# Kernel tuning notes

Hardware: AMD Instinct MI355X
Metric: run time of the kernel (lower is better)

The kernel has to match this reference:

```python
import jax, jax.numpy as jnp
import numpy as np

EMBED = 512
HEADS = 8
HEAD_DIM = EMBED // HEADS
N, S = 4, 2048


def setup_inputs() -> dict:
    key = jax.random.key(0)
    ks = jax.random.split(key, 10)
    value = jax.random.normal(ks[0], (N, S, EMBED), dtype=jnp.float32)
    k_in = jax.random.normal(ks[1], (N, S, EMBED), dtype=jnp.float32)
    q_in = jax.random.normal(ks[2], (N, S, EMBED), dtype=jnp.float32)
    mask = jax.random.randint(ks[3], (N, 1, S, S), 0, 2, dtype=jnp.int32)
    s = 1.0 / np.sqrt(HEAD_DIM)
    Wq = jax.random.uniform(ks[4], (HEAD_DIM, HEAD_DIM), minval=-s, maxval=s, dtype=jnp.float32)
    Wk = jax.random.uniform(ks[5], (HEAD_DIM, HEAD_DIM), minval=-s, maxval=s, dtype=jnp.float32)
    Wv = jax.random.uniform(ks[6], (HEAD_DIM, HEAD_DIM), minval=-s, maxval=s, dtype=jnp.float32)
    so = 1.0 / np.sqrt(EMBED)
    Wo = jax.random.uniform(ks[7], (EMBED, EMBED), minval=-so, maxval=so, dtype=jnp.float32)
    bo = jax.random.uniform(ks[8], (EMBED,), minval=-so, maxval=so, dtype=jnp.float32)
    return {"value": value, "key": k_in, "query": q_in, "mask": mask,
            "Wq": Wq, "Wk": Wk, "Wv": Wv, "Wo": Wo, "bo": bo}


def reference(value, key, query, mask, Wq, Wk, Wv, Wo, bo):
    n, qlen = query.shape[0], query.shape[1]
    # split heads: (N, L, H, D)
    v = value.reshape(n, -1, HEADS, HEAD_DIM)
    k = key.reshape(n, -1, HEADS, HEAD_DIM)
    q = query.reshape(n, qlen, HEADS, HEAD_DIM)
    # per-head linear projections (torch Linear: x @ W^T, no bias)
    v = jnp.einsum('nlhd,ed->nlhe', v, Wv)
    k = jnp.einsum('nlhd,ed->nlhe', k, Wk)
    q = jnp.einsum('nqhd,ed->nqhe', q, Wq)
    # energy: (N, H, Q, K)
    energy = jnp.einsum('nqhd,nkhd->nhqk', q, k)
    energy = jnp.where(mask == 0, jnp.float32(-1e20), energy)
    # NOTE: original scales by sqrt(embed_size), not sqrt(head_dim)
    attn = jax.nn.softmax(energy / jnp.sqrt(jnp.float32(EMBED)), axis=3)
    out = jnp.einsum('nhql,nlhd->nqhd', attn, v).reshape(n, qlen, EMBED)
    return out @ Wo.T + bo
```

## Files before the change

### kernel.cpp

```cpp
#include <hip/hip_runtime.h>

typedef short short8 __attribute__((ext_vector_type(8)));
typedef float f32x4 __attribute__((ext_vector_type(4)));
typedef unsigned short ushort4v __attribute__((ext_vector_type(4)));
typedef unsigned long long u64;
typedef u64 u64x2 __attribute__((ext_vector_type(2)));

#define N_B   4
#define S_LEN 2048
#define EMB   512
#define HD    64
#define NHB   32
#define QSCALE 0.063758714f

#define EXP2F(x) __builtin_amdgcn_exp2f(x)

__device__ unsigned short g_Wqb[64*64];
__device__ unsigned short g_Wkb[64*64];
__device__ unsigned short g_Wvb[64*64];
__device__ unsigned short g_Wob[512*512];
__device__ unsigned short g_Qp[NHB*S_LEN*HD];
__device__ unsigned short g_Kp[NHB*S_LEN*HD];
__device__ unsigned short g_Vt[NHB*HD*S_LEN];
__device__ unsigned short g_AO[N_B*S_LEN*EMB];
__device__ u64            g_Mb[N_B*32*S_LEN];

__device__ __forceinline__ unsigned short f2bf(float f) {
  unsigned u = __float_as_uint(f);
  u = u + 0x7fffu + ((u >> 16) & 1u);
  return (unsigned short)(u >> 16);
}

__device__ __forceinline__ unsigned cvt_pk_bf16(float a, float b) {
  unsigned r;
  asm("v_cvt_pk_bf16_f32 %0, %1, %2" : "=v"(r) : "v"(a), "v"(b));
  return r;
}

__global__ __launch_bounds__(256) void k0_wconv(const float* __restrict__ Wq,
                                                const float* __restrict__ Wk,
                                                const float* __restrict__ Wv,
                                                const float* __restrict__ Wo) {
  int idx = blockIdx.x * 256 + threadIdx.x;
  if (idx < 4096)        g_Wqb[idx]         = f2bf(Wq[idx] * QSCALE);
  else if (idx < 8192)   g_Wkb[idx - 4096]  = f2bf(Wk[idx - 4096]);
  else if (idx < 12288)  g_Wvb[idx - 8192]  = f2bf(Wv[idx - 8192]);
  else                   g_Wob[idx - 12288] = f2bf(Wo[idx - 12288]);
}

__global__ __launch_bounds__(256) void k0b_mask(const int* __restrict__ mask) {
  int wid = blockIdx.x * 4 + (threadIdx.x >> 6);
  int lane = threadIdx.x & 63;
  int n = wid >> 11, q = wid & 2047;
  const int* base = mask + ((size_t)(n * 2048 + q) << 11);
  u64* dst = g_Mb + (size_t)n * 32 * S_LEN + q;
#pragma unroll 4
  for (int j = 0; j < 32; ++j) {
    int mk = base[j * 64 + lane];
    u64 bits = __ballot(mk != 0);
    if (lane == 0) dst[(size_t)j * S_LEN] = bits;
  }
}

__global__ __launch_bounds__(256) void k1_proj(const float* __restrict__ q_in,
                                               const float* __restrict__ k_in,
                                               const float* __restrict__ v_in) {
  __shared__ unsigned short VtL[64][72];
  const int tid = threadIdx.x;
  const int w = tid >> 6, lane = tid & 63, g = lane >> 4, c = lane & 15;
  const int s0 = blockIdx.x * 64;
  const int nh = blockIdx.y, n = nh >> 3, h = nh & 7;
  const int which = blockIdx.z;
  const float* src = which == 0 ? q_in : (which == 1 ? k_in : v_in);
  const unsigned short* Wb = which == 0 ? g_Wqb : (which == 1 ? g_Wkb : g_Wvb);

  short8 xb[2];
  const int srow = s0 + w * 16 + c;
#pragma unroll
  for (int ks = 0; ks < 2; ++ks) {
    const float* ap = src + ((size_t)n * S_LEN + srow) * EMB + h * HD + ks * 32 + g * 8;
    f32x4 x0 = *(const f32x4*)ap;
    f32x4 x1 = *(const f32x4*)(ap + 4);
    short8 tt;
    tt[0] = (short)f2bf(x0[0]); tt[1] = (short)f2bf(x0[1]);
    tt[2] = (short)f2bf(x0[2]); tt[3] = (short)f2bf(x0[3]);
    tt[4] = (short)f2bf(x1[0]); tt[5] = (short)f2bf(x1[1]);
    tt[6] = (short)f2bf(x1[2]); tt[7] = (short)f2bf(x1[3]);
    xb[ks] = tt;
  }

  f32x4 acc[4];
#pragma unroll
  for (int dt = 0; dt < 4; ++dt) { acc[dt][0]=0.f; acc[dt][1]=0.f; acc[dt][2]=0.f; acc[dt][3]=0.f; }

#pragma unroll
  for (int ks = 0; ks < 2; ++ks)
#pragma unroll
    for (int dt = 0; dt < 4; ++dt) {
      short8 a = *(const short8*)(Wb + (dt * 16 + c) * HD + ks * 32 + g * 8);
      acc[dt] = __builtin_amdgcn_mfma_f32_16x16x32_bf16(a, xb[ks], acc[dt], 0, 0, 0);
    }

  if (which < 2) {
    unsigned short* dst = which == 0 ? g_Qp : g_Kp;
#pragma unroll
    for (int dt = 0; dt < 4; ++dt) {
      ushort4v u;
      u[0] = f2bf(acc[dt][0]); u[1] = f2bf(acc[dt][1]);
      u[2] = f2bf(acc[dt][2]); u[3] = f2bf(acc[dt][3]);
      *(ushort4v*)(dst + ((size_t)nh * S_LEN + srow) * HD + dt * 16 + 4 * g) = u;
    }
  } else {
#pragma unroll
    for (int dt = 0; dt < 4; ++dt)
#pragma unroll
      for (int r = 0; r < 4; ++r)
        VtL[dt * 16 + 4 * g + r][w * 16 + c] = f2bf(acc[dt][r]);
    __syncthreads();
#pragma unroll
    for (int rep = 0; rep < 2; ++rep) {
      int cid = tid + rep * 256;
      int row = cid >> 3, ch = cid & 7;
      short8 v = *(const short8*)(&VtL[row][ch * 8]);
      *(short8*)(g_Vt + ((size_t)nh * HD + row) * S_LEN + s0 + ch * 8) = v;
    }
  }
}

__global__ __launch_bounds__(512) void k2_attn() {
  __shared__ unsigned short Kl[2][64][64];
  __shared__ unsigned short Vl[2][80][64];
  __shared__ unsigned short Pl[8][16][64];
  const int tid = threadIdx.x;
  const int w = tid >> 6, lane = tid & 63, g = lane >> 4, c = lane & 15;
  const int q0 = blockIdx.x * 128;
  const int nh = blockIdx.y, n = nh >> 3;

  short8 aq[2];
#pragma unroll
  for (int ks = 0; ks < 2; ++ks)
    aq[ks] = *(const short8*)(g_Qp + ((size_t)nh * S_LEN + q0 + w * 16 + c) * HD + ks * 32 + g * 8);

  const int strow = tid >> 3, schunk = tid & 7;
  const int sdst = (schunk ^ (strow & 7)) * 8;
  const unsigned short* ksrc = g_Kp + ((size_t)nh * S_LEN + strow) * HD + schunk * 8;
  const unsigned short* vsrc = g_Vt + ((size_t)nh * HD + strow) * S_LEN + schunk * 8;
  const u64* mbase = g_Mb + ((size_t)n * 32) * S_LEN + q0 + w * 16 + 4 * g;

  {
    int flat = tid * 4;
    int b = flat >> 10, rem = flat & 1023, rr = rem >> 6, cc = rem & 63;
    ushort4v ones4 = {0x3f80, 0x3f80, 0x3f80, 0x3f80};
    *(ushort4v*)(&Vl[b][64 + rr][cc]) = ones4;
  }

  f32x4 O4[4], O5;
#pragma unroll
  for (int dt = 0; dt < 4; ++dt) { O4[dt][0]=0.f; O4[dt][1]=0.f; O4[dt][2]=0.f; O4[dt][3]=0.f; }
  O5[0]=0.f; O5[1]=0.f; O5[2]=0.f; O5[3]=0.f;

  short8 kst = *(const short8*)(ksrc);
  short8 vst = *(const short8*)(vsrc);
  u64x2 mA = *(const u64x2*)(mbase);
  u64x2 mB = *(const u64x2*)(mbase + 2);
  *(short8*)(&Kl[0][strow][sdst]) = kst;
  *(short8*)(&Vl[0][strow][sdst]) = vst;
  __syncthreads();

  for (int t = 0; t < 32; ++t) {
    const int cur = t & 1;
    u64x2 mAn, mBn;
    if (t < 31) {
      kst = *(const short8*)(ksrc + (size_t)(t + 1) * 64 * HD);
      vst = *(const short8*)(vsrc + (t + 1) * 64);
      mAn = *(const u64x2*)(mbase + (size_t)(t + 1) * S_LEN);
      mBn = *(const u64x2*)(mbase + (size_t)(t + 1) * S_LEN + 2);
    }

    f32x4 sa[4];
#pragma unroll
    for (int ct = 0; ct < 4; ++ct) { sa[ct][0]=0.f; sa[ct][1]=0.f; sa[ct][2]=0.f; sa[ct][3]=0.f; }
#pragma unroll
    for (int ks = 0; ks < 2; ++ks)
#pragma unroll
      for (int ct = 0; ct < 4; ++ct) {
        short8 bk = *(const short8*)(&Kl[cur][ct * 16 + c][((g + 4 * ks) ^ (c & 7)) * 8]);
        sa[ct] = __builtin_amdgcn_mfma_f32_16x16x32_bf16(aq[ks], bk, sa[ct], 0, 0, 0);
      }

    unsigned lo0 = (unsigned)mA[0], hi0 = (unsigned)(mA[0] >> 32);
    unsigned lo1 = (unsigned)mA[1], hi1 = (unsigned)(mA[1] >> 32);
    unsigned lo2 = (unsigned)mB[0], hi2 = (unsigned)(mB[0] >> 32);
    unsigned lo3 = (unsigned)mB[1], hi3 = (unsigned)(mB[1] >> 32);
#pragma unroll
    for (int ct = 0; ct < 4; ++ct) {
      const int sh = (ct & 1) * 16 + c;
      float p0 = ((((ct & 2) ? hi0 : lo0) >> sh) & 1u) ? EXP2F(sa[ct][0]) : 0.f;
      float p1 = ((((ct & 2) ? hi1 : lo1) >> sh) & 1u) ? EXP2F(sa[ct][1]) : 0.f;
      float p2 = ((((ct & 2) ? hi2 : lo2) >> sh) & 1u) ? EXP2F(sa[ct][2]) : 0.f;
      float p3 = ((((ct & 2) ? hi3 : lo3) >> sh) & 1u) ? EXP2F(sa[ct][3]) : 0.f;
      unsigned pk01 = cvt_pk_bf16(p0, p1);
      unsigned pk23 = cvt_pk_bf16(p2, p3);
      const int col = ct * 16 + c;
      const int chs = ((col >> 3) << 3);
#pragma unroll
      for (int r = 0; r < 4; ++r) {
        int prow = 4 * g + r;
        unsigned pk = (r < 2) ? pk01 : pk23;
        unsigned short v = (r & 1) ? (unsigned short)(pk >> 16) : (unsigned short)pk;
        Pl[w][prow][(chs ^ ((prow & 7) << 3)) | (col & 7)] = v;
      }
    }

#pragma unroll
    for (int ks = 0; ks < 2; ++ks) {
      short8 pa = *(const short8*)(&Pl[w][c][((g + 4 * ks) ^ (c & 7)) * 8]);
#pragma unroll
      for (int dt = 0; dt < 5; ++dt) {
        short8 bv = *(const short8*)(&Vl[cur][dt * 16 + c][((g + 4 * ks) ^ (c & 7)) * 8]);
        if (dt < 4)
          O4[dt] = __builtin_amdgcn_mfma_f32_16x16x32_bf16(pa, bv, O4[dt], 0, 0, 0);
        else
          O5 = __builtin_amdgcn_mfma_f32_16x16x32_bf16(pa, bv, O5, 0, 0, 0);
      }
    }

    if (t < 31) {
      *(short8*)(&Kl[cur ^ 1][strow][sdst]) = kst;
      *(short8*)(&Vl[cur ^ 1][strow][sdst]) = vst;
      mA = mAn; mB = mBn;
      __syncthreads();
    }
  }

  const int h = nh & 7;
#pragma unroll
  for (int r = 0; r < 4; ++r) {
    float inv = O5[r] > 0.f ? 1.f / O5[r] : 0.f;
    int qr = q0 + w * 16 + 4 * g + r;
#pragma unroll
    for (int dt = 0; dt < 4; ++dt)
      g_AO[((size_t)n * S_LEN + qr) * EMB + h * HD + dt * 16 + c] = f2bf(O4[dt][r] * inv);
  }
}

__global__ __launch_bounds__(256) void k3_oproj(const float* __restrict__ bo,
                                                float* __restrict__ out) {
  const int tid = threadIdx.x;
  const int w = tid >> 6, lane = tid & 63, g = lane >> 4, c = lane & 15;
  const int m0 = blockIdx.x * 64;
  const int n0 = blockIdx.y * 64;

  f32x4 acc[4];
#pragma unroll
  for (int ct = 0; ct < 4; ++ct) { acc[ct][0]=0.f; acc[ct][1]=0.f; acc[ct][2]=0.f; acc[ct][3]=0.f; }

  for (int ks = 0; ks < 16; ++ks) {
    short8 a = *(const short8*)(g_AO + ((size_t)(m0 + w * 16 + c)) * EMB + ks * 32 + g * 8);
#pragma unroll
    for (int ct = 0; ct < 4; ++ct) {
      short8 b = *(const short8*)(g_Wob + (size_t)(n0 + ct * 16 + c) * EMB + ks * 32 + g * 8);
      acc[ct] = __builtin_amdgcn_mfma_f32_16x16x32_bf16(a, b, acc[ct], 0, 0, 0);
    }
  }

#pragma unroll
  for (int ct = 0; ct < 4; ++ct) {
    int col = n0 + ct * 16 + c;
    float bias = bo[col];
#pragma unroll
    for (int r = 0; r < 4; ++r) {
      int row = m0 + w * 16 + 4 * g + r;
      out[(size_t)row * EMB + col] = acc[ct][r] + bias;
    }
  }
}

extern "C" void kernel_launch(void* const* d_in, const int* in_sizes, int n_in,
                              void* d_out, int out_size, void* d_ws, size_t ws_size,
                              hipStream_t stream) {
  const float* value = (const float*)d_in[0];
  const float* key   = (const float*)d_in[1];
  const float* query = (const float*)d_in[2];
  const int*   mask  = (const int*)d_in[3];
  const float* Wq    = (const float*)d_in[4];
  const float* Wk    = (const float*)d_in[5];
  const float* Wv    = (const float*)d_in[6];
  const float* Wo    = (const float*)d_in[7];
  const float* bo    = (const float*)d_in[8];
  float* out = (float*)d_out;

  k0_wconv<<<1072, 256, 0, stream>>>(Wq, Wk, Wv, Wo);
  k0b_mask<<<2048, 256, 0, stream>>>(mask);
  k1_proj<<<dim3(32, 32, 3), 256, 0, stream>>>(query, key, value);
  k2_attn<<<dim3(16, 32), 512, 0, stream>>>();
  k3_oproj<<<dim3(128, 8), 256, 0, stream>>>(bo, out);
}
```

Baseline: 273.4 us.

## Rewrite attention with 32x32 MFMA, in-register P, and split-KV halves

The attention kernel now uses 32x32x16 bf16 MFMA. The probability tile stays in registers, exchanged across lanes with shuffles instead of a shared-memory round trip. The row sum is accumulated directly rather than through an extra ones-column MFMA. The two halves of the block's waves each process half of the key range, and their partial outputs are combined through LDS at the end. The weight and mask prep kernels are merged into a single launch, and the projection kernel now loops over all heads per block so the weight fragments are reused. This trades more registers and an LDS reduction for fewer LDS writes and fewer MFMA instructions in the hot loop.

```diff
diff --git a/kernel.cpp b/kernel.cpp
--- a/kernel.cpp
+++ b/kernel.cpp
@@ -2,9 +2,10 @@
 
 typedef short short8 __attribute__((ext_vector_type(8)));
 typedef float f32x4 __attribute__((ext_vector_type(4)));
+typedef float f32x16 __attribute__((ext_vector_type(16)));
 typedef unsigned short ushort4v __attribute__((ext_vector_type(4)));
+typedef unsigned int uint4v __attribute__((ext_vector_type(4)));
 typedef unsigned long long u64;
-typedef u64 u64x2 __attribute__((ext_vector_type(2)));
 
 #define N_B   4
 #define S_LEN 2048
@@ -12,7 +13,6 @@
 #define HD    64
 #define NHB   32
 #define QSCALE 0.063758714f
-
 #define EXP2F(x) __builtin_amdgcn_exp2f(x)
 
 __device__ unsigned short g_Wqb[64*64];
@@ -30,35 +30,36 @@
   u = u + 0x7fffu + ((u >> 16) & 1u);
   return (unsigned short)(u >> 16);
 }
-
 __device__ __forceinline__ unsigned cvt_pk_bf16(float a, float b) {
   unsigned r;
   asm("v_cvt_pk_bf16_f32 %0, %1, %2" : "=v"(r) : "v"(a), "v"(b));
   return r;
 }
 
-__global__ __launch_bounds__(256) void k0_wconv(const float* __restrict__ Wq,
-                                                const float* __restrict__ Wk,
-                                                const float* __restrict__ Wv,
-                                                const float* __restrict__ Wo) {
-  int idx = blockIdx.x * 256 + threadIdx.x;
-  if (idx < 4096)        g_Wqb[idx]         = f2bf(Wq[idx] * QSCALE);
-  else if (idx < 8192)   g_Wkb[idx - 4096]  = f2bf(Wk[idx - 4096]);
-  else if (idx < 12288)  g_Wvb[idx - 8192]  = f2bf(Wv[idx - 8192]);
-  else                   g_Wob[idx - 12288] = f2bf(Wo[idx - 12288]);
-}
-
-__global__ __launch_bounds__(256) void k0b_mask(const int* __restrict__ mask) {
-  int wid = blockIdx.x * 4 + (threadIdx.x >> 6);
-  int lane = threadIdx.x & 63;
-  int n = wid >> 11, q = wid & 2047;
-  const int* base = mask + ((size_t)(n * 2048 + q) << 11);
-  u64* dst = g_Mb + (size_t)n * 32 * S_LEN + q;
+__global__ __launch_bounds__(256) void k0_prep(const float* __restrict__ Wq,
+                                               const float* __restrict__ Wk,
+                                               const float* __restrict__ Wv,
+                                               const float* __restrict__ Wo,
+                                               const int* __restrict__ mask) {
+  const int b = blockIdx.x;
+  if (b < 1072) {
+    int idx = b * 256 + threadIdx.x;
+    if (idx < 4096)        g_Wqb[idx]         = f2bf(Wq[idx] * QSCALE);
+    else if (idx < 8192)   g_Wkb[idx - 4096]  = f2bf(Wk[idx - 4096]);
+    else if (idx < 12288)  g_Wvb[idx - 8192]  = f2bf(Wv[idx - 8192]);
+    else                   g_Wob[idx - 12288] = f2bf(Wo[idx - 12288]);
+  } else {
+    int wid = (b - 1072) * 4 + (threadIdx.x >> 6);
+    int lane = threadIdx.x & 63;
+    int n = wid >> 11, q = wid & 2047;
+    const int* base = mask + ((size_t)(n * 2048 + q) << 11);
+    u64* dst = g_Mb + (size_t)n * 32 * S_LEN + q;
 #pragma unroll 4
-  for (int j = 0; j < 32; ++j) {
-    int mk = base[j * 64 + lane];
-    u64 bits = __ballot(mk != 0);
-    if (lane == 0) dst[(size_t)j * S_LEN] = bits;
+    for (int j = 0; j < 32; ++j) {
+      int mk = base[j * 64 + lane];
+      u64 bits = __ballot(mk != 0);
+      if (lane == 0) dst[(size_t)j * S_LEN] = bits;
+    }
   }
 }
 
@@ -69,178 +70,221 @@
   const int tid = threadIdx.x;
   const int w = tid >> 6, lane = tid & 63, g = lane >> 4, c = lane & 15;
   const int s0 = blockIdx.x * 64;
-  const int nh = blockIdx.y, n = nh >> 3, h = nh & 7;
+  const int n = blockIdx.y;
   const int which = blockIdx.z;
   const float* src = which == 0 ? q_in : (which == 1 ? k_in : v_in);
   const unsigned short* Wb = which == 0 ? g_Wqb : (which == 1 ? g_Wkb : g_Wvb);
 
-  short8 xb[2];
   const int srow = s0 + w * 16 + c;
-#pragma unroll
-  for (int ks = 0; ks < 2; ++ks) {
-    const float* ap = src + ((size_t)n * S_LEN + srow) * EMB + h * HD + ks * 32 + g * 8;
-    f32x4 x0 = *(const f32x4*)ap;
-    f32x4 x1 = *(const f32x4*)(ap + 4);
-    short8 tt;
-    tt[0] = (short)f2bf(x0[0]); tt[1] = (short)f2bf(x0[1]);
-    tt[2] = (short)f2bf(x0[2]); tt[3] = (short)f2bf(x0[3]);
-    tt[4] = (short)f2bf(x1[0]); tt[5] = (short)f2bf(x1[1]);
-    tt[6] = (short)f2bf(x1[2]); tt[7] = (short)f2bf(x1[3]);
-    xb[ks] = tt;
-  }
-
-  f32x4 acc[4];
-#pragma unroll
-  for (int dt = 0; dt < 4; ++dt) { acc[dt][0]=0.f; acc[dt][1]=0.f; acc[dt][2]=0.f; acc[dt][3]=0.f; }
-
+  const float* rowp = src + ((size_t)n * S_LEN + srow) * EMB;
+
+  short8 wf[2][4];
 #pragma unroll
   for (int ks = 0; ks < 2; ++ks)
 #pragma unroll
-    for (int dt = 0; dt < 4; ++dt) {
-      short8 a = *(const short8*)(Wb + (dt * 16 + c) * HD + ks * 32 + g * 8);
-      acc[dt] = __builtin_amdgcn_mfma_f32_16x16x32_bf16(a, xb[ks], acc[dt], 0, 0, 0);
-    }
-
-  if (which < 2) {
-    unsigned short* dst = which == 0 ? g_Qp : g_Kp;
-#pragma unroll
-    for (int dt = 0; dt < 4; ++dt) {
-      ushort4v u;
-      u[0] = f2bf(acc[dt][0]); u[1] = f2bf(acc[dt][1]);
-      u[2] = f2bf(acc[dt][2]); u[3] = f2bf(acc[dt][3]);
-      *(ushort4v*)(dst + ((size_t)nh * S_LEN + srow) * HD + dt * 16 + 4 * g) = u;
-    }
-  } else {
-#pragma unroll
     for (int dt = 0; dt < 4; ++dt)
-#pragma unroll
-      for (int r = 0; r < 4; ++r)
-        VtL[dt * 16 + 4 * g + r][w * 16 + c] = f2bf(acc[dt][r]);
+      wf[ks][dt] = *(const short8*)(Wb + (dt * 16 + c) * HD + ks * 32 + g * 8);
+
+  for (int hd = 0; hd < 8; ++hd) {
+    short8 xb[2];
+#pragma unroll
+    for (int ks = 0; ks < 2; ++ks) {
+      const float* ap = rowp + hd * HD + ks * 32 + g * 8;
+      f32x4 x0 = *(const f32x4*)ap;
+      f32x4 x1 = *(const f32x4*)(ap + 4);
+      short8 tt;
+      tt[0] = (short)f2bf(x0[0]); tt[1] = (short)f2bf(x0[1]);
+      tt[2] = (short)f2bf(x0[2]); tt[3] = (short)f2bf(x0[3]);
+      tt[4] = (short)f2bf(x1[0]); tt[5] = (short)f2bf(x1[1]);
+      tt[6] = (short)f2bf(x1[2]); tt[7] = (short)f2bf(x1[3]);
+      xb[ks] = tt;
+    }
+    f32x4 acc[4];
+#pragma unroll
+    for (int dt = 0; dt < 4; ++dt) { acc[dt][0]=0.f; acc[dt][1]=0.f; acc[dt][2]=0.f; acc[dt][3]=0.f; }
+#pragma unroll
+    for (int ks = 0; ks < 2; ++ks)
+#pragma unroll
+      for (int dt = 0; dt < 4; ++dt)
+        acc[dt] = __builtin_amdgcn_mfma_f32_16x16x32_bf16(wf[ks][dt], xb[ks], acc[dt], 0, 0, 0);
+
+    const int nh = n * 8 + hd;
+    if (which < 2) {
+      unsigned short* dst = which == 0 ? g_Qp : g_Kp;
+#pragma unroll
+      for (int dt = 0; dt < 4; ++dt) {
+        ushort4v u;
+        u[0] = f2bf(acc[dt][0]); u[1] = f2bf(acc[dt][1]);
+        u[2] = f2bf(acc[dt][2]); u[3] = f2bf(acc[dt][3]);
+        *(ushort4v*)(dst + ((size_t)nh * S_LEN + srow) * HD + dt * 16 + 4 * g) = u;
+      }
+    } else {
+      if (hd) __syncthreads();
+#pragma unroll
+      for (int dt = 0; dt < 4; ++dt)
+#pragma unroll
+        for (int r = 0; r < 4; ++r)
+          VtL[dt * 16 + 4 * g + r][w * 16 + c] = f2bf(acc[dt][r]);
+      __syncthreads();
+#pragma unroll
+      for (int rep = 0; rep < 2; ++rep) {
+        int cid = tid + rep * 256;
+        int row = cid >> 3, ch = cid & 7;
+        short8 v = *(const short8*)(&VtL[row][ch * 8]);
+        *(short8*)(g_Vt + ((size_t)nh * HD + row) * S_LEN + s0 + ch * 8) = v;
+      }
+    }
+  }
+}
+
+__global__ __launch_bounds__(512, 4) void k2_attn() {
+  __shared__ alignas(16) unsigned short Kl[2][2][64][64];
+  __shared__ alignas(16) unsigned short Vl[2][2][64][64];
+  const int tid = threadIdx.x;
+  const int w = tid >> 6, lane = tid & 63;
+  const int q32 = lane & 31, hh = lane >> 5;
+  const int half = w >> 2;
+  const int q0 = blockIdx.x * 128;
+  const int nh = blockIdx.y, n = nh >> 3, h = nh & 7;
+  const int qrow = q0 + (w & 3) * 32 + q32;
+
+  short8 qf[4];
+#pragma unroll
+  for (int ks = 0; ks < 4; ++ks)
+    qf[ks] = *(const short8*)(g_Qp + ((size_t)nh * S_LEN + qrow) * HD + ks * 16 + hh * 8);
+
+  const int th = tid & 255;
+  const int srow = th >> 2;
+  const int scp = (th & 3) * 2;
+  const unsigned short* ksrc = g_Kp + ((size_t)nh * S_LEN + half * 1024 + srow) * HD + scp * 8;
+  const unsigned short* vsrc = g_Vt + ((size_t)nh * HD + srow) * S_LEN + half * 1024 + scp * 8;
+  const int kd0 = ((scp) ^ (srow & 7)) * 8;
+  const int kd1 = ((scp + 1) ^ (srow & 7)) * 8;
+  const u64* mptr = g_Mb + ((size_t)n * 32 + half * 16) * S_LEN + qrow;
+
+  f32x16 O0, O1;
+#pragma unroll
+  for (int i = 0; i < 16; ++i) { O0[i] = 0.f; O1[i] = 0.f; }
+  float ld = 0.f;
+
+  short8 ka0 = *(const short8*)(ksrc);
+  short8 ka1 = *(const short8*)(ksrc + 8);
+  short8 va0 = *(const short8*)(vsrc);
+  short8 va1 = *(const short8*)(vsrc + 8);
+  u64 mcur = mptr[0];
+  *(short8*)(&Kl[half][0][srow][kd0]) = ka0;
+  *(short8*)(&Kl[half][0][srow][kd1]) = ka1;
+  *(short8*)(&Vl[half][0][srow][kd0]) = va0;
+  *(short8*)(&Vl[half][0][srow][kd1]) = va1;
+  __syncthreads();
+
+  for (int tl = 0; tl < 16; ++tl) {
+    const int cur = tl & 1;
+    u64 mnext = 0;
+    if (tl < 15) {
+      ka0 = *(const short8*)(ksrc + (size_t)(tl + 1) * 4096);
+      ka1 = *(const short8*)(ksrc + (size_t)(tl + 1) * 4096 + 8);
+      va0 = *(const short8*)(vsrc + (tl + 1) * 64);
+      va1 = *(const short8*)(vsrc + (tl + 1) * 64 + 8);
+      mnext = mptr[(size_t)(tl + 1) * S_LEN];
+    }
+
+    unsigned cL[16];
+    float psum = 0.f;
+#pragma unroll
+    for (int st = 0; st < 2; ++st) {
+      f32x16 sa;
+#pragma unroll
+      for (int i = 0; i < 16; ++i) sa[i] = 0.f;
+      const int arow = st * 32 + q32;
+#pragma unroll
+      for (int ks = 0; ks < 4; ++ks) {
+        short8 ka = *(const short8*)(&Kl[half][cur][arow][((2 * ks + hh) ^ (arow & 7)) * 8]);
+        sa = __builtin_amdgcn_mfma_f32_32x32x16_bf16(ka, qf[ks], sa, 0, 0, 0);
+      }
+      unsigned mw = st ? (unsigned)(mcur >> 32) : (unsigned)mcur;
+      const int shb = 4 * hh;
+#pragma unroll
+      for (int j2 = 0; j2 < 4; ++j2) {
+        float p0 = ((mw >> (8 * j2 + shb + 0)) & 1u) ? EXP2F(sa[4 * j2 + 0]) : 0.f;
+        float p1 = ((mw >> (8 * j2 + shb + 1)) & 1u) ? EXP2F(sa[4 * j2 + 1]) : 0.f;
+        float p2 = ((mw >> (8 * j2 + shb + 2)) & 1u) ? EXP2F(sa[4 * j2 + 2]) : 0.f;
+        float p3 = ((mw >> (8 * j2 + shb + 3)) & 1u) ? EXP2F(sa[4 * j2 + 3]) : 0.f;
+        psum += (p0 + p1) + (p2 + p3);
+        cL[st * 8 + 2 * j2]     = cvt_pk_bf16(p0, p1);
+        cL[st * 8 + 2 * j2 + 1] = cvt_pk_bf16(p2, p3);
+      }
+    }
+    ld += psum + __shfl_xor(psum, 32);
+
+#pragma unroll
+    for (int ks = 0; ks < 4; ++ks) {
+      unsigned s0v = __shfl_xor(cL[4 * ks + 0], 32);
+      unsigned s1v = __shfl_xor(cL[4 * ks + 1], 32);
+      unsigned s2v = __shfl_xor(cL[4 * ks + 2], 32);
+      unsigned s3v = __shfl_xor(cL[4 * ks + 3], 32);
+      uint4v fv;
+      fv[0] = hh ? s2v : cL[4 * ks + 0];
+      fv[1] = hh ? s3v : cL[4 * ks + 1];
+      fv[2] = hh ? cL[4 * ks + 2] : s0v;
+      fv[3] = hh ? cL[4 * ks + 3] : s1v;
+      short8 pa = __builtin_bit_cast(short8, fv);
+      const int vr0 = q32;
+      short8 vb0 = *(const short8*)(&Vl[half][cur][vr0][((2 * ks + hh) ^ (vr0 & 7)) * 8]);
+      O0 = __builtin_amdgcn_mfma_f32_32x32x16_bf16(pa, vb0, O0, 0, 0, 0);
+      const int vr1 = 32 + q32;
+      short8 vb1 = *(const short8*)(&Vl[half][cur][vr1][((2 * ks + hh) ^ (vr1 & 7)) * 8]);
+      O1 = __builtin_amdgcn_mfma_f32_32x32x16_bf16(pa, vb1, O1, 0, 0, 0);
+    }
+
+    if (tl < 15) {
+      *(short8*)(&Kl[half][cur ^ 1][srow][kd0]) = ka0;
+      *(short8*)(&Kl[half][cur ^ 1][srow][kd1]) = ka1;
+      *(short8*)(&Vl[half][cur ^ 1][srow][kd0]) = va0;
+      *(short8*)(&Vl[half][cur ^ 1][srow][kd1]) = va1;
+      mcur = mnext;
+    }
     __syncthreads();
-#pragma unroll
-    for (int rep = 0; rep < 2; ++rep) {
-      int cid = tid + rep * 256;
-      int row = cid >> 3, ch = cid & 7;
-      short8 v = *(const short8*)(&VtL[row][ch * 8]);
-      *(short8*)(g_Vt + ((size_t)nh * HD + row) * S_LEN + s0 + ch * 8) = v;
-    }
-  }
-}
-
-__global__ __launch_bounds__(512) void k2_attn() {
-  __shared__ unsigned short Kl[2][64][64];
-  __shared__ unsigned short Vl[2][80][64];
-  __shared__ unsigned short Pl[8][16][64];
-  const int tid = threadIdx.x;
-  const int w = tid >> 6, lane = tid & 63, g = lane >> 4, c = lane & 15;
-  const int q0 = blockIdx.x * 128;
-  const int nh = blockIdx.y, n = nh >> 3;
-
-  short8 aq[2];
-#pragma unroll
-  for (int ks = 0; ks < 2; ++ks)
-    aq[ks] = *(const short8*)(g_Qp + ((size_t)nh * S_LEN + q0 + w * 16 + c) * HD + ks * 32 + g * 8);
-
-  const int strow = tid >> 3, schunk = tid & 7;
-  const int sdst = (schunk ^ (strow & 7)) * 8;
-  const unsigned short* ksrc = g_Kp + ((size_t)nh * S_LEN + strow) * HD + schunk * 8;
-  const unsigned short* vsrc = g_Vt + ((size_t)nh * HD + strow) * S_LEN + schunk * 8;
-  const u64* mbase = g_Mb + ((size_t)n * 32) * S_LEN + q0 + w * 16 + 4 * g;
-
+  }
+
+  float* Olds = (float*)&Kl[0][0][0][0];
+  float* Lsum = (float*)&Vl[0][0][0][0];
+  const int qb = (w & 3) * 32;
+  if (half == 0) {
+#pragma unroll
+    for (int r = 0; r < 16; ++r) {
+      int qq = qb + (r & 3) + 8 * (r >> 2) + 4 * hh;
+      Olds[qq * 64 + q32]      = O0[r];
+      Olds[qq * 64 + 32 + q32] = O1[r];
+    }
+    if (hh == 0) Lsum[qb + q32] = ld;
+  }
+  __syncthreads();
+  if (half == 1) {
+#pragma unroll
+    for (int r = 0; r < 16; ++r) {
+      int qq = qb + (r & 3) + 8 * (r >> 2) + 4 * hh;
+      Olds[qq * 64 + q32]      += O0[r];
+      Olds[qq * 64 + 32 + q32] += O1[r];
+    }
+    if (hh == 0) Lsum[qb + q32] += ld;
+  }
+  __syncthreads();
   {
-    int flat = tid * 4;
-    int b = flat >> 10, rem = flat & 1023, rr = rem >> 6, cc = rem & 63;
-    ushort4v ones4 = {0x3f80, 0x3f80, 0x3f80, 0x3f80};
-    *(ushort4v*)(&Vl[b][64 + rr][cc]) = ones4;
-  }
-
-  f32x4 O4[4], O5;
-#pragma unroll
-  for (int dt = 0; dt < 4; ++dt) { O4[dt][0]=0.f; O4[dt][1]=0.f; O4[dt][2]=0.f; O4[dt][3]=0.f; }
-  O5[0]=0.f; O5[1]=0.f; O5[2]=0.f; O5[3]=0.f;
-
-  short8 kst = *(const short8*)(ksrc);
-  short8 vst = *(const short8*)(vsrc);
-  u64x2 mA = *(const u64x2*)(mbase);
-  u64x2 mB = *(const u64x2*)(mbase + 2);
-  *(short8*)(&Kl[0][strow][sdst]) = kst;
-  *(short8*)(&Vl[0][strow][sdst]) = vst;
-  __syncthreads();
-
-  for (int t = 0; t < 32; ++t) {
-    const int cur = t & 1;
-    u64x2 mAn, mBn;
-    if (t < 31) {
-      kst = *(const short8*)(ksrc + (size_t)(t + 1) * 64 * HD);
-      vst = *(const short8*)(vsrc + (t + 1) * 64);
-      mAn = *(const u64x2*)(mbase + (size_t)(t + 1) * S_LEN);
-      mBn = *(const u64x2*)(mbase + (size_t)(t + 1) * S_LEN + 2);
-    }
-
-    f32x4 sa[4];
-#pragma unroll
-    for (int ct = 0; ct < 4; ++ct) { sa[ct][0]=0.f; sa[ct][1]=0.f; sa[ct][2]=0.f; sa[ct][3]=0.f; }
-#pragma unroll
-    for (int ks = 0; ks < 2; ++ks)
-#pragma unroll
-      for (int ct = 0; ct < 4; ++ct) {
-        short8 bk = *(const short8*)(&Kl[cur][ct * 16 + c][((g + 4 * ks) ^ (c & 7)) * 8]);
-        sa[ct] = __builtin_amdgcn_mfma_f32_16x16x32_bf16(aq[ks], bk, sa[ct], 0, 0, 0);
-      }
-
-    unsigned lo0 = (unsigned)mA[0], hi0 = (unsigned)(mA[0] >> 32);
-    unsigned lo1 = (unsigned)mA[1], hi1 = (unsigned)(mA[1] >> 32);
-    unsigned lo2 = (unsigned)mB[0], hi2 = (unsigned)(mB[0] >> 32);
-    unsigned lo3 = (unsigned)mB[1], hi3 = (unsigned)(mB[1] >> 32);
-#pragma unroll
-    for (int ct = 0; ct < 4; ++ct) {
-      const int sh = (ct & 1) * 16 + c;
-      float p0 = ((((ct & 2) ? hi0 : lo0) >> sh) & 1u) ? EXP2F(sa[ct][0]) : 0.f;
-      float p1 = ((((ct & 2) ? hi1 : lo1) >> sh) & 1u) ? EXP2F(sa[ct][1]) : 0.f;
-      float p2 = ((((ct & 2) ? hi2 : lo2) >> sh) & 1u) ? EXP2F(sa[ct][2]) : 0.f;
-      float p3 = ((((ct & 2) ? hi3 : lo3) >> sh) & 1u) ? EXP2F(sa[ct][3]) : 0.f;
-      unsigned pk01 = cvt_pk_bf16(p0, p1);
-      unsigned pk23 = cvt_pk_bf16(p2, p3);
-      const int col = ct * 16 + c;
-      const int chs = ((col >> 3) << 3);
-#pragma unroll
-      for (int r = 0; r < 4; ++r) {
-        int prow = 4 * g + r;
-        unsigned pk = (r < 2) ? pk01 : pk23;
-        unsigned short v = (r & 1) ? (unsigned short)(pk >> 16) : (unsigned short)pk;
-        Pl[w][prow][(chs ^ ((prow & 7) << 3)) | (col & 7)] = v;
-      }
-    }
-
-#pragma unroll
-    for (int ks = 0; ks < 2; ++ks) {
-      short8 pa = *(const short8*)(&Pl[w][c][((g + 4 * ks) ^ (c & 7)) * 8]);
-#pragma unroll
-      for (int dt = 0; dt < 5; ++dt) {
-        short8 bv = *(const short8*)(&Vl[cur][dt * 16 + c][((g + 4 * ks) ^ (c & 7)) * 8]);
-        if (dt < 4)
-          O4[dt] = __builtin_amdgcn_mfma_f32_16x16x32_bf16(pa, bv, O4[dt], 0, 0, 0);
-        else
-          O5 = __builtin_amdgcn_mfma_f32_16x16x32_bf16(pa, bv, O5, 0, 0, 0);
-      }
-    }
-
-    if (t < 31) {
-      *(short8*)(&Kl[cur ^ 1][strow][sdst]) = kst;
-      *(short8*)(&Vl[cur ^ 1][strow][sdst]) = vst;
-      mA = mAn; mB = mBn;
-      __syncthreads();
-    }
-  }
-
-  const int h = nh & 7;
-#pragma unroll
-  for (int r = 0; r < 4; ++r) {
-    float inv = O5[r] > 0.f ? 1.f / O5[r] : 0.f;
-    int qr = q0 + w * 16 + 4 * g + r;
-#pragma unroll
-    for (int dt = 0; dt < 4; ++dt)
-      g_AO[((size_t)n * S_LEN + qr) * EMB + h * HD + dt * 16 + c] = f2bf(O4[dt][r] * inv);
+    const int rr = tid >> 2;
+    const int dch = (tid & 3) * 16;
+    float l = Lsum[rr];
+    float inv = l > 0.f ? 1.f / l : 0.f;
+    const float* op = &Olds[rr * 64 + dch];
+    unsigned pk[8];
+#pragma unroll
+    for (int j = 0; j < 8; ++j)
+      pk[j] = cvt_pk_bf16(op[2 * j] * inv, op[2 * j + 1] * inv);
+    uint4v lo4 = {pk[0], pk[1], pk[2], pk[3]};
+    uint4v hi4 = {pk[4], pk[5], pk[6], pk[7]};
+    unsigned short* dst = g_AO + ((size_t)n * S_LEN + q0 + rr) * EMB + h * HD + dch;
+    *(short8*)(dst)     = __builtin_bit_cast(short8, lo4);
+    *(short8*)(dst + 8) = __builtin_bit_cast(short8, hi4);
   }
 }
 
@@ -290,9 +334,8 @@
   const float* bo    = (const float*)d_in[8];
   float* out = (float*)d_out;
 
-  k0_wconv<<<1072, 256, 0, stream>>>(Wq, Wk, Wv, Wo);
-  k0b_mask<<<2048, 256, 0, stream>>>(mask);
-  k1_proj<<<dim3(32, 32, 3), 256, 0, stream>>>(query, key, value);
+  k0_prep<<<3120, 256, 0, stream>>>(Wq, Wk, Wv, Wo, mask);
+  k1_proj<<<dim3(32, 4, 3), 256, 0, stream>>>(query, key, value);
   k2_attn<<<dim3(16, 32), 512, 0, stream>>>();
   k3_oproj<<<dim3(128, 8), 256, 0, stream>>>(bo, out);
 }
```

New measurement: 336.1 us. 1.23x slower.
